# Optimization experiments

Measured on AMD Instinct MI355X. Metric: run time of the kernel, lower is better.

## Reference

```python
import jax, jax.numpy as jnp
import numpy as np

E = 500_000   # total flattened ngram-node occurrences
N = 100_000   # nr_cfg_nodes
D = 256       # cfg_node_encoding_dim


def setup_inputs() -> dict:
    key = jax.random.key(0)
    ks = jax.random.split(key, 6)
    scattered_input = jax.random.normal(ks[0], (E, D), dtype=jnp.float32)
    previous_cfg_nodes_encodings = jax.random.normal(ks[1], (N, D), dtype=jnp.float32)
    W_k = jax.random.normal(ks[2], (D, D), dtype=jnp.float32) / np.float32(np.sqrt(D))
    b_k = jnp.zeros((D,), dtype=jnp.float32)
    W_g = jax.random.normal(ks[3], (2 * D, D), dtype=jnp.float32) / np.float32(np.sqrt(2 * D))
    b_g = jnp.zeros((D,), dtype=jnp.float32)
    indices = jax.random.randint(ks[4], (E,), 0, N, dtype=jnp.int32)
    return {
        "scattered_input": scattered_input,
        "previous_cfg_nodes_encodings": previous_cfg_nodes_encodings,
        "W_k": W_k, "b_k": b_k, "W_g": W_g, "b_g": b_g,
        "indices": indices,
        "nr_cfg_nodes": N,
    }


def reference(scattered_input, previous_cfg_nodes_encodings, W_k, b_k, W_g, b_g, indices, nr_cfg_nodes):
    d = scattered_input.shape[-1]
    # --- ScatterCombiner, method='attn': scatter-softmax attention per CFG node ---
    keys = scattered_input @ W_k + b_k                       # [E, D]
    queries = previous_cfg_nodes_encodings[indices]          # [E, D] gather per occurrence
    scores = jnp.sum(keys * queries, axis=-1) * (1.0 / jnp.sqrt(jnp.float32(d)))  # [E]
    seg_max = jax.ops.segment_max(scores, indices, num_segments=nr_cfg_nodes)     # [N]
    seg_max = jnp.where(jnp.isfinite(seg_max), seg_max, jnp.float32(0.0))         # empty segments
    ex = jnp.exp(scores - seg_max[indices])                  # [E]
    denom = jax.ops.segment_sum(ex, indices, num_segments=nr_cfg_nodes)           # [N]
    probs = ex / jnp.maximum(denom[indices], jnp.float32(1e-9))                   # [E]
    combined = jax.ops.segment_sum(probs[:, None] * scattered_input, indices,
                                   num_segments=nr_cfg_nodes)                     # [N, D]
    # --- StateUpdater: GRU-like sigmoid gate (dropout disabled / eval mode) ---
    gate_in = jnp.concatenate([previous_cfg_nodes_encodings, combined], axis=-1)  # [N, 2D]
    gate = jax.nn.sigmoid(gate_in @ W_g + b_g)               # [N, D]
    return gate * previous_cfg_nodes_encodings + (1.0 - gate) * combined
```

## Files before the change

### kernel.cpp

```cpp
#include <hip/hip_runtime.h>
#include <math.h>

#define D 256

typedef __attribute__((ext_vector_type(8))) short short8;
typedef __attribute__((ext_vector_type(4))) float f32x4;

__device__ inline unsigned short f2bf(float f) {
    unsigned int u = __float_as_uint(f);
    u += 0x7fff + ((u >> 16) & 1);
    return (unsigned short)(u >> 16);
}
__device__ inline float bf2f(unsigned short h) {
    return __uint_as_float(((unsigned int)h) << 16);
}

__global__ __launch_bounds__(256)
void k_cvt(const float* __restrict__ in, unsigned short* __restrict__ out, int n8) {
    int i = blockIdx.x * 256 + threadIdx.x;
    if (i >= n8) return;
    const float4* p = (const float4*)(in + (size_t)i * 8);
    float4 a = p[0], b = p[1];
    ushort4 o0 = { f2bf(a.x), f2bf(a.y), f2bf(a.z), f2bf(a.w) };
    ushort4 o1 = { f2bf(b.x), f2bf(b.y), f2bf(b.z), f2bf(b.w) };
    ushort4* q = (ushort4*)(out + (size_t)i * 8);
    q[0] = o0; q[1] = o1;
}

__global__ __launch_bounds__(256)
void k_cvt_wg(const float* __restrict__ Wg, unsigned short* __restrict__ WgT) {
    int r = blockIdx.x;
    int c = threadIdx.x;
    WgT[(size_t)c * (2 * D) + r] = f2bf(Wg[(size_t)r * D + c]);
}

template <int K, bool GATE>
__global__ __launch_bounds__(256)
void k_mfma_gemm(const unsigned short* __restrict__ A0,
                 const unsigned short* __restrict__ A1,
                 const unsigned short* __restrict__ Bn,
                 const float* __restrict__ bg,
                 const float* __restrict__ prevf,
                 unsigned short* __restrict__ wq_out,
                 float* __restrict__ outp,
                 int Nrows) {
    __shared__ unsigned short As[64 * 32];
    __shared__ unsigned short Bs[256 * 32];

    int tid  = threadIdx.x;
    int wave = tid >> 6;
    int lane = tid & 63;
    int lcol = lane & 15;
    int quad = lane >> 4;
    int row0 = blockIdx.x * 64;

    f32x4 acc[4][4];
    #pragma unroll
    for (int i = 0; i < 4; i++)
        #pragma unroll
        for (int j = 0; j < 4; j++) acc[i][j] = (f32x4){0.f, 0.f, 0.f, 0.f};

    int arow = tid >> 2, ako = (tid & 3) * 8;
    int grow = row0 + arow;

    for (int kk = 0; kk < K; kk += 32) {
        const unsigned short* Asrc = A0;
        int kc = kk;
        if (GATE && kk >= 256) { Asrc = A1; kc = kk - 256; }

        uint4 av = make_uint4(0u, 0u, 0u, 0u);
        if (grow < Nrows) av = *(const uint4*)&Asrc[(size_t)grow * D + kc + ako];
        *(uint4*)&As[arow * 32 + ako] = av;

        #pragma unroll
        for (int i = 0; i < 4; i++) {
            int c = tid + i * 256;
            int brow = c >> 2, bko = (c & 3) * 8;
            *(uint4*)&Bs[brow * 32 + bko] =
                *(const uint4*)&Bn[(size_t)brow * K + kk + bko];
        }
        __syncthreads();

        short8 a[4], b[4];
        #pragma unroll
        for (int mf = 0; mf < 4; mf++)
            a[mf] = *(const short8*)&As[(mf * 16 + lcol) * 32 + quad * 8];
        #pragma unroll
        for (int nf = 0; nf < 4; nf++)
            b[nf] = *(const short8*)&Bs[(wave * 64 + nf * 16 + lcol) * 32 + quad * 8];
        #pragma unroll
        for (int mf = 0; mf < 4; mf++)
            #pragma unroll
            for (int nf = 0; nf < 4; nf++)
                acc[mf][nf] = __builtin_amdgcn_mfma_f32_16x16x32_bf16(
                    a[mf], b[nf], acc[mf][nf], 0, 0, 0);
        __syncthreads();
    }

    if (!GATE) {
        #pragma unroll
        for (int mf = 0; mf < 4; mf++) {
            #pragma unroll
            for (int nf = 0; nf < 4; nf++) {
                int col = wave * 64 + nf * 16 + lcol;
                #pragma unroll
                for (int r = 0; r < 4; r++) {
                    int gr = row0 + mf * 16 + quad * 4 + r;
                    if (gr < Nrows)
                        wq_out[(size_t)gr * D + col] = f2bf(acc[mf][nf][r]);
                }
            }
        }
    } else {
        float bgv[4];
        #pragma unroll
        for (int nf = 0; nf < 4; nf++) bgv[nf] = bg[wave * 64 + nf * 16 + lcol];
        #pragma unroll
        for (int mf = 0; mf < 4; mf++) {
            #pragma unroll
            for (int nf = 0; nf < 4; nf++) {
                int col = wave * 64 + nf * 16 + lcol;
                #pragma unroll
                for (int r = 0; r < 4; r++) {
                    int gr = row0 + mf * 16 + quad * 4 + r;
                    if (gr < Nrows) {
                        size_t o = (size_t)gr * D + col;
                        float logit = acc[mf][nf][r] + bgv[nf];
                        float g = 1.f / (1.f + __expf(-logit));
                        float cb = bf2f(A1[o]);
                        outp[o] = g * prevf[o] + (1.f - g) * cb;
                    }
                }
            }
        }
    }
}

__global__ __launch_bounds__(256)
void k_zero(int* __restrict__ p, int n) {
    int i = blockIdx.x * 256 + threadIdx.x;
    if (i < n) p[i] = 0;
}

__global__ __launch_bounds__(256)
void k_hist(const int* __restrict__ idx, int* __restrict__ counts,
            int* __restrict__ rank, int E_) {
    int e = blockIdx.x * 256 + threadIdx.x;
    if (e < E_) rank[e] = atomicAdd(&counts[idx[e]], 1);
}

__global__ __launch_bounds__(256)
void k_part(const int* __restrict__ counts, int* __restrict__ chunkSums, int Nn) {
    __shared__ int sd[256];
    int base = blockIdx.x * 1024;
    int t = threadIdx.x;
    int s = 0;
    #pragma unroll
    for (int i = 0; i < 4; i++) {
        int g = base + t + i * 256;
        if (g < Nn) s += counts[g];
    }
    sd[t] = s;
    __syncthreads();
    for (int st = 128; st; st >>= 1) {
        if (t < st) sd[t] += sd[t + st];
        __syncthreads();
    }
    if (t == 0) chunkSums[blockIdx.x] = sd[0];
}

__global__ __launch_bounds__(256)
void k_top(const int* __restrict__ cs, int* __restrict__ co, int P,
           int* __restrict__ offsets, int Nn, int E_) {
    __shared__ int carry;
    __shared__ int ws[4];
    int t = threadIdx.x, lane = t & 63, w = t >> 6;
    if (t == 0) carry = 0;
    __syncthreads();
    for (int base = 0; base < P; base += 256) {
        int i = base + t;
        int v = (i < P) ? cs[i] : 0;
        int orig = v;
        for (int off = 1; off < 64; off <<= 1) {
            int u = __shfl_up(v, off, 64);
            if (lane >= off) v += u;
        }
        if (lane == 63) ws[w] = v;
        __syncthreads();
        int wex = 0;
        for (int k = 0; k < w; k++) wex += ws[k];
        int incl = v + wex;
        if (i < P) co[i] = carry + incl - orig;
        __syncthreads();
        if (t == 255) carry += incl;
        __syncthreads();
    }
    if (t == 0) offsets[Nn] = E_;
}

__global__ __launch_bounds__(256)
void k_off(const int* __restrict__ counts, const int* __restrict__ chunkOff,
           int* __restrict__ offsets, int Nn) {
    int t = threadIdx.x, lane = t & 63, w = t >> 6;
    int base = blockIdx.x * 1024 + t * 4;
    int c[4]; int ts = 0;
    #pragma unroll
    for (int j = 0; j < 4; j++) {
        int g = base + j;
        c[j] = (g < Nn) ? counts[g] : 0;
        ts += c[j];
    }
    int v = ts;
    for (int off = 1; off < 64; off <<= 1) {
        int u = __shfl_up(v, off, 64);
        if (lane >= off) v += u;
    }
    __shared__ int ws[4];
    if (lane == 63) ws[w] = v;
    __syncthreads();
    int wex = 0;
    for (int k = 0; k < w; k++) wex += ws[k];
    int run = chunkOff[blockIdx.x] + wex + v - ts;
    #pragma unroll
    for (int j = 0; j < 4; j++) {
        int g = base + j;
        if (g < Nn) offsets[g] = run;
        run += c[j];
    }
}

__global__ __launch_bounds__(256)
void k_scatter(const int* __restrict__ idx, const int* __restrict__ rank,
               const int* __restrict__ offsets, int* __restrict__ perm, int E_) {
    int e = blockIdx.x * 256 + threadIdx.x;
    if (e < E_) perm[offsets[idx[e]] + rank[e]] = e;
}

__global__ __launch_bounds__(256)
void k_combine(const float* __restrict__ scat, const unsigned short* __restrict__ wq,
               const int* __restrict__ offsets, const int* __restrict__ perm,
               unsigned short* __restrict__ comb, int Nnodes) {
    int wave = threadIdx.x >> 6;
    int lane = threadIdx.x & 63;
    int n = blockIdx.x * 4 + wave;
    if (n >= Nnodes) return;

    ushort4 wu = *(const ushort4*)&wq[(size_t)n * D + lane * 4];
    float4 wqv = { bf2f(wu.x), bf2f(wu.y), bf2f(wu.z), bf2f(wu.w) };
    int beg = offsets[n], end = offsets[n + 1];

    float m = -INFINITY, l = 0.f;
    float4 acc = { 0.f, 0.f, 0.f, 0.f };
    const float scale = 0.0625f;

    if (beg < end) {
        int e = perm[beg];
        float4 sv = *(const float4*)&scat[(size_t)e * D + lane * 4];
        for (int pos = beg; pos < end; ++pos) {
            float4 cur = sv;
            if (pos + 1 < end) {
                int e2 = perm[pos + 1];
                sv = *(const float4*)&scat[(size_t)e2 * D + lane * 4];
            }
            float d = fmaf(cur.x, wqv.x, fmaf(cur.y, wqv.y,
                      fmaf(cur.z, wqv.z, cur.w * wqv.w)));
            #pragma unroll
            for (int off = 32; off; off >>= 1) d += __shfl_xor(d, off, 64);
            float score = d * scale;
            float nm = fmaxf(m, score);
            float al = __expf(m - nm);
            float p  = __expf(score - nm);
            l = fmaf(l, al, p);
            acc.x = fmaf(acc.x, al, p * cur.x);
            acc.y = fmaf(acc.y, al, p * cur.y);
            acc.z = fmaf(acc.z, al, p * cur.z);
            acc.w = fmaf(acc.w, al, p * cur.w);
            m = nm;
        }
    }
    float inv = 1.f / fmaxf(l, 1e-9f);
    ushort4 o = { f2bf(acc.x * inv), f2bf(acc.y * inv),
                  f2bf(acc.z * inv), f2bf(acc.w * inv) };
    *(ushort4*)&comb[(size_t)n * D + lane * 4] = o;
}

extern "C" void kernel_launch(void* const* d_in, const int* in_sizes, int n_in,
                              void* d_out, int out_size, void* d_ws, size_t ws_size,
                              hipStream_t stream) {
    const float* scat = (const float*)d_in[0];
    const float* prev = (const float*)d_in[1];
    const float* Wk   = (const float*)d_in[2];
    const float* Wg   = (const float*)d_in[4];
    const float* bg   = (const float*)d_in[5];
    const int*   idx  = (const int*)d_in[6];

    const int E_ = in_sizes[6];
    const int Nn = in_sizes[1] / D;

    float* out = (float*)d_out;

    char* w = (char*)d_ws;
    auto alloc = [&](size_t bytes) -> char* {
        char* p = w;
        w += (bytes + 255) & ~(size_t)255;
        return p;
    };
    unsigned short* prev_bf = (unsigned short*)alloc((size_t)Nn * D * 2);
    unsigned short* wq_bf   = (unsigned short*)alloc((size_t)Nn * D * 2);
    unsigned short* comb_bf = (unsigned short*)alloc((size_t)Nn * D * 2);
    unsigned short* Wk_bf   = (unsigned short*)alloc((size_t)D * D * 2);
    unsigned short* WgT_bf  = (unsigned short*)alloc((size_t)2 * D * D * 2);
    int*   counts    = (int*)alloc((size_t)Nn * 4);
    int*   offsets   = (int*)alloc(((size_t)Nn + 1) * 4);
    int    P         = (Nn + 1023) / 1024;
    int*   chunkSums = (int*)alloc((size_t)P * 4);
    int*   chunkOff  = (int*)alloc((size_t)P * 4);
    int*   rank      = (int*)alloc((size_t)E_ * 4);
    int*   perm      = (int*)alloc((size_t)E_ * 4);

    int n8 = Nn * D / 8;
    k_cvt<<<(n8 + 255) / 256, 256, 0, stream>>>(prev, prev_bf, n8);
    k_cvt<<<(D * D / 8 + 255) / 256, 256, 0, stream>>>(Wk, Wk_bf, D * D / 8);
    k_cvt_wg<<<2 * D, D, 0, stream>>>(Wg, WgT_bf);

    k_zero<<<(Nn + 255) / 256, 256, 0, stream>>>(counts, Nn);
    int gb = (E_ + 255) / 256;
    k_hist<<<gb, 256, 0, stream>>>(idx, counts, rank, E_);
    k_part<<<P, 256, 0, stream>>>(counts, chunkSums, Nn);
    k_top<<<1, 256, 0, stream>>>(chunkSums, chunkOff, P, offsets, Nn, E_);
    k_off<<<P, 256, 0, stream>>>(counts, chunkOff, offsets, Nn);
    k_scatter<<<gb, 256, 0, stream>>>(idx, rank, offsets, perm, E_);

    int gm = (Nn + 63) / 64;
    k_mfma_gemm<256, false><<<gm, 256, 0, stream>>>(
        prev_bf, nullptr, Wk_bf, nullptr, nullptr, wq_bf, nullptr, Nn);

    k_combine<<<(Nn + 3) / 4, 256, 0, stream>>>(scat, wq_bf, offsets, perm, comb_bf, Nn);

    k_mfma_gemm<512, true><<<gm, 256, 0, stream>>>(
        prev_bf, comb_bf, WgT_bf, bg, prev, nullptr, out, Nn);
}
```

Before: 1.012 ms.

## Fuse prep kernels, pad GEMM LDS rows, deepen combine prefetch

Merges the three conversion kernels and the counts zeroing into one launch so fewer kernels are dispatched. Pads the GEMM shared-memory row stride from 32 to 40 elements to reduce LDS bank conflicts on the MFMA operand reads. Extends the gather prefetch in the segment-attention combine loop to two rows ahead to hide more global-load latency. The cost is slightly more LDS use and more registers per lane in the combine kernel.

New measurement: 998.5 us. Within noise of the previous version (-1.3%).

```diff
diff --git a/kernel.cpp b/kernel.cpp
--- a/kernel.cpp
+++ b/kernel.cpp
@@ -2,6 +2,7 @@
 #include <math.h>
 
 #define D 256
+#define LDS_STRIDE 40
 
 typedef __attribute__((ext_vector_type(8))) short short8;
 typedef __attribute__((ext_vector_type(4))) float f32x4;
@@ -16,22 +17,41 @@
 }
 
 __global__ __launch_bounds__(256)
-void k_cvt(const float* __restrict__ in, unsigned short* __restrict__ out, int n8) {
-    int i = blockIdx.x * 256 + threadIdx.x;
-    if (i >= n8) return;
-    const float4* p = (const float4*)(in + (size_t)i * 8);
-    float4 a = p[0], b = p[1];
-    ushort4 o0 = { f2bf(a.x), f2bf(a.y), f2bf(a.z), f2bf(a.w) };
-    ushort4 o1 = { f2bf(b.x), f2bf(b.y), f2bf(b.z), f2bf(b.w) };
-    ushort4* q = (ushort4*)(out + (size_t)i * 8);
-    q[0] = o0; q[1] = o1;
-}
-
-__global__ __launch_bounds__(256)
-void k_cvt_wg(const float* __restrict__ Wg, unsigned short* __restrict__ WgT) {
-    int r = blockIdx.x;
-    int c = threadIdx.x;
-    WgT[(size_t)c * (2 * D) + r] = f2bf(Wg[(size_t)r * D + c]);
+void k_prep(const float* __restrict__ prev, const float* __restrict__ Wk,
+            const float* __restrict__ Wg,
+            unsigned short* __restrict__ prev_bf, unsigned short* __restrict__ Wk_bf,
+            unsigned short* __restrict__ WgT, int* __restrict__ counts,
+            int n8, int nWk8, int Nn, int gPrev, int gWk, int gWgT) {
+    int b = blockIdx.x;
+    int t = threadIdx.x;
+    if (b < gPrev) {
+        int i = b * 256 + t;
+        if (i < n8) {
+            const float4* p = (const float4*)(prev + (size_t)i * 8);
+            float4 a = p[0], c = p[1];
+            ushort4 o0 = { f2bf(a.x), f2bf(a.y), f2bf(a.z), f2bf(a.w) };
+            ushort4 o1 = { f2bf(c.x), f2bf(c.y), f2bf(c.z), f2bf(c.w) };
+            ushort4* q = (ushort4*)(prev_bf + (size_t)i * 8);
+            q[0] = o0; q[1] = o1;
+        }
+    } else if (b < gPrev + gWk) {
+        int i = (b - gPrev) * 256 + t;
+        if (i < nWk8) {
+            const float4* p = (const float4*)(Wk + (size_t)i * 8);
+            float4 a = p[0], c = p[1];
+            ushort4 o0 = { f2bf(a.x), f2bf(a.y), f2bf(a.z), f2bf(a.w) };
+            ushort4 o1 = { f2bf(c.x), f2bf(c.y), f2bf(c.z), f2bf(c.w) };
+            ushort4* q = (ushort4*)(Wk_bf + (size_t)i * 8);
+            q[0] = o0; q[1] = o1;
+        }
+    } else if (b < gPrev + gWk + gWgT) {
+        int r = b - gPrev - gWk;
+        int c = t;
+        WgT[(size_t)c * (2 * D) + r] = f2bf(Wg[(size_t)r * D + c]);
+    } else {
+        int i = (b - gPrev - gWk - gWgT) * 256 + t;
+        if (i < Nn) counts[i] = 0;
+    }
 }
 
 template <int K, bool GATE>
@@ -44,8 +64,8 @@
                  unsigned short* __restrict__ wq_out,
                  float* __restrict__ outp,
                  int Nrows) {
-    __shared__ unsigned short As[64 * 32];
-    __shared__ unsigned short Bs[256 * 32];
+    __shared__ unsigned short As[64 * LDS_STRIDE];
+    __shared__ unsigned short Bs[256 * LDS_STRIDE];
 
     int tid  = threadIdx.x;
     int wave = tid >> 6;
@@ -70,13 +90,13 @@
 
         uint4 av = make_uint4(0u, 0u, 0u, 0u);
         if (grow < Nrows) av = *(const uint4*)&Asrc[(size_t)grow * D + kc + ako];
-        *(uint4*)&As[arow * 32 + ako] = av;
+        *(uint4*)&As[arow * LDS_STRIDE + ako] = av;
 
         #pragma unroll
         for (int i = 0; i < 4; i++) {
             int c = tid + i * 256;
             int brow = c >> 2, bko = (c & 3) * 8;
-            *(uint4*)&Bs[brow * 32 + bko] =
+            *(uint4*)&Bs[brow * LDS_STRIDE + bko] =
                 *(const uint4*)&Bn[(size_t)brow * K + kk + bko];
         }
         __syncthreads();
@@ -84,10 +104,10 @@
         short8 a[4], b[4];
         #pragma unroll
         for (int mf = 0; mf < 4; mf++)
-            a[mf] = *(const short8*)&As[(mf * 16 + lcol) * 32 + quad * 8];
+            a[mf] = *(const short8*)&As[(mf * 16 + lcol) * LDS_STRIDE + quad * 8];
         #pragma unroll
         for (int nf = 0; nf < 4; nf++)
-            b[nf] = *(const short8*)&Bs[(wave * 64 + nf * 16 + lcol) * 32 + quad * 8];
+            b[nf] = *(const short8*)&Bs[(wave * 64 + nf * 16 + lcol) * LDS_STRIDE + quad * 8];
         #pragma unroll
         for (int mf = 0; mf < 4; mf++)
             #pragma unroll
@@ -137,12 +157,6 @@
 }
 
 __global__ __launch_bounds__(256)
-void k_zero(int* __restrict__ p, int n) {
-    int i = blockIdx.x * 256 + threadIdx.x;
-    if (i < n) p[i] = 0;
-}
-
-__global__ __launch_bounds__(256)
 void k_hist(const int* __restrict__ idx, int* __restrict__ counts,
             int* __restrict__ rank, int E_) {
     int e = blockIdx.x * 256 + threadIdx.x;
@@ -254,13 +268,19 @@
     const float scale = 0.0625f;
 
     if (beg < end) {
-        int e = perm[beg];
-        float4 sv = *(const float4*)&scat[(size_t)e * D + lane * 4];
+        int e0 = perm[beg];
+        float4 sv0 = *(const float4*)&scat[(size_t)e0 * D + lane * 4];
+        float4 sv1 = sv0;
+        if (beg + 1 < end) {
+            int e1 = perm[beg + 1];
+            sv1 = *(const float4*)&scat[(size_t)e1 * D + lane * 4];
+        }
         for (int pos = beg; pos < end; ++pos) {
-            float4 cur = sv;
-            if (pos + 1 < end) {
-                int e2 = perm[pos + 1];
-                sv = *(const float4*)&scat[(size_t)e2 * D + lane * 4];
+            float4 cur = sv0;
+            sv0 = sv1;
+            if (pos + 2 < end) {
+                int e2 = perm[pos + 2];
+                sv1 = *(const float4*)&scat[(size_t)e2 * D + lane * 4];
             }
             float d = fmaf(cur.x, wqv.x, fmaf(cur.y, wqv.y,
                       fmaf(cur.z, wqv.z, cur.w * wqv.w)));
@@ -318,12 +338,16 @@
     int*   rank      = (int*)alloc((size_t)E_ * 4);
     int*   perm      = (int*)alloc((size_t)E_ * 4);
 
-    int n8 = Nn * D / 8;
-    k_cvt<<<(n8 + 255) / 256, 256, 0, stream>>>(prev, prev_bf, n8);
-    k_cvt<<<(D * D / 8 + 255) / 256, 256, 0, stream>>>(Wk, Wk_bf, D * D / 8);
-    k_cvt_wg<<<2 * D, D, 0, stream>>>(Wg, WgT_bf);
-
-    k_zero<<<(Nn + 255) / 256, 256, 0, stream>>>(counts, Nn);
+    int n8    = Nn * D / 8;
+    int nWk8  = D * D / 8;
+    int gPrev = (n8 + 255) / 256;
+    int gWk   = (nWk8 + 255) / 256;
+    int gWgT  = 2 * D;
+    int gCnt  = (Nn + 255) / 256;
+    k_prep<<<gPrev + gWk + gWgT + gCnt, 256, 0, stream>>>(
+        prev, Wk, Wg, prev_bf, Wk_bf, WgT_bf, counts,
+        n8, nWk8, Nn, gPrev, gWk, gWgT);
+
     int gb = (E_ + 255) / 256;
     k_hist<<<gb, 256, 0, stream>>>(idx, counts, rank, E_);
     k_part<<<P, 256, 0, stream>>>(counts, chunkSums, Nn);
```
